# Optimization experiments

Hardware: AMD Instinct MI355X
Metric: run time of the kernel (lower is better)

## Reference

```python
import jax, jax.numpy as jnp
import numpy as np
from jax import lax

SPARSE_TH = 0.01
STRIDE = (1, 1)


def setup_inputs() -> dict:
    key = jax.random.key(0)
    k1, k2, k3 = jax.random.split(key, 3)
    x = jax.random.normal(k1, (32, 56, 56, 256), dtype=jnp.float32)  # NHWC
    # weight: (out_channels, in_channels, kh, kw); scale so a fraction falls below sparse_th
    weight = jax.random.normal(k2, (256, 256, 3, 3), dtype=jnp.float32) * 0.05
    bias = jax.random.normal(k3, (256,), dtype=jnp.float32)
    return {"x": x, "weight": weight, "bias": bias}


def reference(x, weight, bias):
    # Threshold weights: |w| < sparse_th -> 0 (the sparse kernel computes the
    # identical math as a dense valid conv with the masked weight)
    w = jnp.where(jnp.abs(weight) < SPARSE_TH, jnp.zeros_like(weight), weight)
    # OIHW -> HWIO for NHWC conv
    w_hwio = jnp.transpose(w, (2, 3, 1, 0))
    out = lax.conv_general_dilated(
        x, w_hwio,
        window_strides=STRIDE,
        padding="VALID",
        dimension_numbers=("NHWC", "HWIO", "NHWC"),
    )
    return out + bias.reshape(1, 1, 1, -1)
```

## Files before the change

kernel.cpp:

```cpp
#include <hip/hip_runtime.h>
#include <hip/hip_bf16.h>


typedef __bf16 bf16x8 __attribute__((ext_vector_type(8)));
typedef float f32x4 __attribute__((ext_vector_type(4)));

#define GLOBAL_AS __attribute__((address_space(1)))
#define LDS_AS __attribute__((address_space(3)))

static __device__ __forceinline__ void glds16(const void* g, void* l) {
    __builtin_amdgcn_global_load_lds((const GLOBAL_AS unsigned int*)g,
                                     (LDS_AS unsigned int*)l, 16, 0, 0);
}

static __device__ __forceinline__ unsigned short f2bf(float f) {
    unsigned int u = __float_as_uint(f);
    unsigned int r = u + 0x7FFFu + ((u >> 16) & 1u);
    return (unsigned short)(r >> 16);
}

__global__ void cvt_x(const float* __restrict__ in, unsigned short* __restrict__ out, int n) {
    int i = (blockIdx.x * 256 + threadIdx.x) * 8;
    if (i >= n) return;
    const float4* p = (const float4*)(in + i);
    float4 a = p[0], b = p[1];
    uint4 v;
    v.x = (unsigned)f2bf(a.x) | ((unsigned)f2bf(a.y) << 16);
    v.y = (unsigned)f2bf(a.z) | ((unsigned)f2bf(a.w) << 16);
    v.z = (unsigned)f2bf(b.x) | ((unsigned)f2bf(b.y) << 16);
    v.w = (unsigned)f2bf(b.z) | ((unsigned)f2bf(b.w) << 16);
    *(uint4*)(out + i) = v;
}

__global__ void cvt_w(const float* __restrict__ w, unsigned short* __restrict__ wt) {
    int co = blockIdx.x;
    int ci = threadIdx.x;
    const float* src = w + co * 2304 + ci * 9;
    unsigned short* dst = wt + co * 2304 + ci;
#pragma unroll
    for (int khw = 0; khw < 9; ++khw) {
        float v = src[khw];
        v = (fabsf(v) < 0.01f) ? 0.0f : v;
        dst[khw * 256] = f2bf(v);
    }
}

static __device__ __forceinline__ int swz_key(int row16) {
    return (row16 & 3) ^ ((row16 >> 2) & 3);
}

__global__ __launch_bounds__(256) void conv_gemm(
    const unsigned short* __restrict__ Xb,
    const unsigned short* __restrict__ Wt,
    const float* __restrict__ bias,
    float* __restrict__ Out)
{
    __shared__ __align__(16) unsigned short As[128 * 32];
    __shared__ __align__(16) unsigned short Bs[128 * 32];

    const int tid  = threadIdx.x;
    const int lane = tid & 63;
    const int wave = tid >> 6;

    const int bx = blockIdx.x;
    const int xcd = bx & 7;
    const int slt = bx >> 3;
    const int v   = xcd * 182 + (xcd < 2 ? xcd : 2) + slt;
    const int m0  = (v >> 1) * 128;
    const int co0 = (v & 1) * 128;

    const int srow = lane >> 2;
    const int schunk_g = (lane & 3) ^ swz_key(srow);
    const int scol = schunk_g * 8;

    const unsigned short* a_src[2];
    const unsigned short* b_src[2];
#pragma unroll
    for (int r = 0; r < 2; ++r) {
        int row = r * 64 + wave * 16 + srow;
        int m = m0 + row;
        int n = m / 2916;
        int rem = m - n * 2916;
        int oh = rem / 54;
        int ow = rem - oh * 54;
        a_src[r] = Xb + (((n * 56 + oh) * 56 + ow) << 8) + scol;
        b_src[r] = Wt + (co0 + row) * 2304 + scol;
    }
    unsigned short* a_dst[2] = { As + wave * 512, As + 2048 + wave * 512 };
    unsigned short* b_dst[2] = { Bs + wave * 512, Bs + 2048 + wave * 512 };

    const int fm = lane & 15;
    const int fq = lane >> 4;
    const int wm = (wave >> 1) * 64;
    const int wn = (wave & 1) * 64;
    const int slot8 = (fq ^ swz_key(fm)) * 8;

    f32x4 acc[4][4];
#pragma unroll
    for (int i = 0; i < 4; ++i)
#pragma unroll
        for (int j = 0; j < 4; ++j)
            acc[i][j] = (f32x4){0.f, 0.f, 0.f, 0.f};

    int kc = 0;
    for (int khw = 0; khw < 9; ++khw) {
        const int kh = khw / 3;
        const int kw = khw - kh * 3;
        const int aoff0 = (kh * 56 + kw) << 8;
#pragma unroll 1
        for (int c = 0; c < 8; ++c, ++kc) {
            const int aoff = aoff0 + c * 32;
            const int boff = kc * 32;
            __syncthreads();
#pragma unroll
            for (int r = 0; r < 2; ++r) {
                glds16(a_src[r] + aoff, a_dst[r]);
                glds16(b_src[r] + boff, b_dst[r]);
            }
            __syncthreads();

            bf16x8 af[4], bfr[4];
#pragma unroll
            for (int mi = 0; mi < 4; ++mi)
                af[mi] = *(const bf16x8*)&As[(wm + mi * 16 + fm) * 32 + slot8];
#pragma unroll
            for (int ni = 0; ni < 4; ++ni)
                bfr[ni] = *(const bf16x8*)&Bs[(wn + ni * 16 + fm) * 32 + slot8];
#pragma unroll
            for (int mi = 0; mi < 4; ++mi)
#pragma unroll
                for (int ni = 0; ni < 4; ++ni)
                    acc[mi][ni] = __builtin_amdgcn_mfma_f32_16x16x32_bf16(
                        af[mi], bfr[ni], acc[mi][ni], 0, 0, 0);
        }
    }

    float bv[4];
#pragma unroll
    for (int ni = 0; ni < 4; ++ni) bv[ni] = bias[co0 + wn + ni * 16 + fm];
#pragma unroll
    for (int mi = 0; mi < 4; ++mi) {
#pragma unroll
        for (int reg = 0; reg < 4; ++reg) {
            int m = m0 + wm + mi * 16 + fq * 4 + reg;
            float* orow = Out + m * 256 + co0 + wn + fm;
#pragma unroll
            for (int ni = 0; ni < 4; ++ni)
                orow[ni * 16] = acc[mi][ni][reg] + bv[ni];
        }
    }
}

extern "C" void kernel_launch(void* const* d_in, const int* in_sizes, int n_in,
                              void* d_out, int out_size, void* d_ws, size_t ws_size,
                              hipStream_t stream) {
    const float* x    = (const float*)d_in[0];
    const float* w    = (const float*)d_in[1];
    const float* bias = (const float*)d_in[2];
    float* out = (float*)d_out;

    const int NX = 32 * 56 * 56 * 256;
    unsigned short* xb = (unsigned short*)d_ws;
    unsigned short* wt = xb + NX;

    cvt_x<<<NX / (256 * 8), 256, 0, stream>>>(x, xb, NX);
    cvt_w<<<256, 256, 0, stream>>>(w, wt);
    conv_gemm<<<729 * 2, 256, 0, stream>>>(xb, wt, bias, out);
}
```

Before: 304.9 us.

## Double-buffer LDS tiles with prefetch and merge conversion kernels

The GEMM main loop moves to two LDS buffers. The next K-chunk is issued with global_load_lds before the MFMAs on the current chunk run, which overlaps global loads with compute and cuts the barriers from two per iteration to one. The separate input and weight bf16 conversion kernels are merged into a single launch, saving one kernel launch. LDS use per block doubles, which may limit occupancy.

```diff
diff --git a/kernel.cpp b/kernel.cpp
--- a/kernel.cpp
+++ b/kernel.cpp
@@ -19,29 +19,30 @@
     return (unsigned short)(r >> 16);
 }
 
-__global__ void cvt_x(const float* __restrict__ in, unsigned short* __restrict__ out, int n) {
-    int i = (blockIdx.x * 256 + threadIdx.x) * 8;
-    if (i >= n) return;
-    const float4* p = (const float4*)(in + i);
-    float4 a = p[0], b = p[1];
-    uint4 v;
-    v.x = (unsigned)f2bf(a.x) | ((unsigned)f2bf(a.y) << 16);
-    v.y = (unsigned)f2bf(a.z) | ((unsigned)f2bf(a.w) << 16);
-    v.z = (unsigned)f2bf(b.x) | ((unsigned)f2bf(b.y) << 16);
-    v.w = (unsigned)f2bf(b.z) | ((unsigned)f2bf(b.w) << 16);
-    *(uint4*)(out + i) = v;
-}
-
-__global__ void cvt_w(const float* __restrict__ w, unsigned short* __restrict__ wt) {
-    int co = blockIdx.x;
-    int ci = threadIdx.x;
-    const float* src = w + co * 2304 + ci * 9;
-    unsigned short* dst = wt + co * 2304 + ci;
+__global__ void cvt_xw(const float* __restrict__ x, unsigned short* __restrict__ xb,
+                       const float* __restrict__ w, unsigned short* __restrict__ wt) {
+    const int NXB = 32 * 56 * 56 * 256 / (256 * 8);
+    if (blockIdx.x < NXB) {
+        int i = (blockIdx.x * 256 + threadIdx.x) * 8;
+        const float4* p = (const float4*)(x + i);
+        float4 a = p[0], b = p[1];
+        uint4 v;
+        v.x = (unsigned)f2bf(a.x) | ((unsigned)f2bf(a.y) << 16);
+        v.y = (unsigned)f2bf(a.z) | ((unsigned)f2bf(a.w) << 16);
+        v.z = (unsigned)f2bf(b.x) | ((unsigned)f2bf(b.y) << 16);
+        v.w = (unsigned)f2bf(b.z) | ((unsigned)f2bf(b.w) << 16);
+        *(uint4*)(xb + i) = v;
+    } else {
+        int co = blockIdx.x - NXB;
+        int ci = threadIdx.x;
+        const float* src = w + co * 2304 + ci * 9;
+        unsigned short* dst = wt + co * 2304 + ci;
 #pragma unroll
-    for (int khw = 0; khw < 9; ++khw) {
-        float v = src[khw];
-        v = (fabsf(v) < 0.01f) ? 0.0f : v;
-        dst[khw * 256] = f2bf(v);
+        for (int khw = 0; khw < 9; ++khw) {
+            float v = src[khw];
+            v = (fabsf(v) < 0.01f) ? 0.0f : v;
+            dst[khw * 256] = f2bf(v);
+        }
     }
 }
 
@@ -55,8 +56,8 @@
     const float* __restrict__ bias,
     float* __restrict__ Out)
 {
-    __shared__ __align__(16) unsigned short As[128 * 32];
-    __shared__ __align__(16) unsigned short Bs[128 * 32];
+    __shared__ __align__(16) unsigned short As[2][128 * 32];
+    __shared__ __align__(16) unsigned short Bs[2][128 * 32];
 
     const int tid  = threadIdx.x;
     const int lane = tid & 63;
@@ -86,8 +87,6 @@
         a_src[r] = Xb + (((n * 56 + oh) * 56 + ow) << 8) + scol;
         b_src[r] = Wt + (co0 + row) * 2304 + scol;
     }
-    unsigned short* a_dst[2] = { As + wave * 512, As + 2048 + wave * 512 };
-    unsigned short* b_dst[2] = { Bs + wave * 512, Bs + 2048 + wave * 512 };
 
     const int fm = lane & 15;
     const int fq = lane >> 4;
@@ -102,37 +101,46 @@
         for (int j = 0; j < 4; ++j)
             acc[i][j] = (f32x4){0.f, 0.f, 0.f, 0.f};
 
-    int kc = 0;
-    for (int khw = 0; khw < 9; ++khw) {
-        const int kh = khw / 3;
-        const int kw = khw - kh * 3;
-        const int aoff0 = (kh * 56 + kw) << 8;
+#pragma unroll
+    for (int r = 0; r < 2; ++r) {
+        glds16(a_src[r], &As[0][wave * 512 + r * 2048]);
+        glds16(b_src[r], &Bs[0][wave * 512 + r * 2048]);
+    }
+
 #pragma unroll 1
-        for (int c = 0; c < 8; ++c, ++kc) {
-            const int aoff = aoff0 + c * 32;
-            const int boff = kc * 32;
-            __syncthreads();
+    for (int kc = 0; kc < 72; ++kc) {
+        __syncthreads();
+
+        if (kc < 71) {
+            const int kcn = kc + 1;
+            const int khwn = kcn >> 3;
+            const int khn = (khwn * 11) >> 5;
+            const int kwn = khwn - khn * 3;
+            const int aoffn = ((khn * 56 + kwn) << 8) + (kcn & 7) * 32;
+            const int boffn = kcn * 32;
+            const int b = kcn & 1;
 #pragma unroll
             for (int r = 0; r < 2; ++r) {
-                glds16(a_src[r] + aoff, a_dst[r]);
-                glds16(b_src[r] + boff, b_dst[r]);
+                glds16(a_src[r] + aoffn, &As[b][wave * 512 + r * 2048]);
+                glds16(b_src[r] + boffn, &Bs[b][wave * 512 + r * 2048]);
             }
-            __syncthreads();
+        }
 
-            bf16x8 af[4], bfr[4];
+        const unsigned short* Ab = As[kc & 1];
+        const unsigned short* Bb = Bs[kc & 1];
+        bf16x8 af[4], bfr[4];
 #pragma unroll
-            for (int mi = 0; mi < 4; ++mi)
-                af[mi] = *(const bf16x8*)&As[(wm + mi * 16 + fm) * 32 + slot8];
+        for (int mi = 0; mi < 4; ++mi)
+            af[mi] = *(const bf16x8*)&Ab[(wm + mi * 16 + fm) * 32 + slot8];
+#pragma unroll
+        for (int ni = 0; ni < 4; ++ni)
+            bfr[ni] = *(const bf16x8*)&Bb[(wn + ni * 16 + fm) * 32 + slot8];
+#pragma unroll
+        for (int mi = 0; mi < 4; ++mi)
 #pragma unroll
             for (int ni = 0; ni < 4; ++ni)
-                bfr[ni] = *(const bf16x8*)&Bs[(wn + ni * 16 + fm) * 32 + slot8];
-#pragma unroll
-            for (int mi = 0; mi < 4; ++mi)
-#pragma unroll
-                for (int ni = 0; ni < 4; ++ni)
-                    acc[mi][ni] = __builtin_amdgcn_mfma_f32_16x16x32_bf16(
-                        af[mi], bfr[ni], acc[mi][ni], 0, 0, 0);
-        }
+                acc[mi][ni] = __builtin_amdgcn_mfma_f32_16x16x32_bf16(
+                    af[mi], bfr[ni], acc[mi][ni], 0, 0, 0);
     }
 
     float bv[4];
@@ -163,7 +171,6 @@
     unsigned short* xb = (unsigned short*)d_ws;
     unsigned short* wt = xb + NX;
 
-    cvt_x<<<NX / (256 * 8), 256, 0, stream>>>(x, xb, NX);
-    cvt_w<<<256, 256, 0, stream>>>(w, wt);
+    cvt_xw<<<NX / (256 * 8) + 256, 256, 0, stream>>>(x, xb, w, wt);
     conv_gemm<<<729 * 2, 256, 0, stream>>>(xb, wt, bias, out);
 }
```

Measured after the change: 302.5 us. No clear change (-0.8%).
